# Optimization experiments

Hardware: AMD Instinct MI355X
Metric: run time of the kernel (lower is better)

The kernel has to match this reference:

```python
import jax, jax.numpy as jnp
import numpy as np

N, E, D, H, K = 100000, 1600000, 512, 256, 64


def setup_inputs() -> dict:
    key = jax.random.key(0)
    ks = jax.random.split(key, 8)
    x = jax.random.normal(ks[0], (N, D), dtype=jnp.float32)
    edge_index = jax.random.randint(ks[1], (2, E), 0, N, dtype=jnp.int64)
    W1 = jax.random.normal(ks[2], (D, H), dtype=jnp.float32) / np.sqrt(D)
    b1 = jnp.zeros((H,), dtype=jnp.float32)
    W2 = jax.random.normal(ks[3], (H, H), dtype=jnp.float32) / np.sqrt(H)
    b2 = jnp.zeros((H,), dtype=jnp.float32)
    Wk = jax.random.normal(ks[4], (H, K), dtype=jnp.float32) / np.sqrt(H)
    log_tau = jnp.array(np.log(1.0), dtype=jnp.float32)
    return {"x": x, "edge_index": edge_index, "W1": W1, "b1": b1,
            "W2": W2, "b2": b2, "Wk": Wk, "log_tau": log_tau}


def _gcn_norm(edge_index, n):
    # add self-loops, compute sym-normalized edge weights (PyG GCNConv default)
    loop = jnp.arange(n, dtype=edge_index.dtype)
    src = jnp.concatenate([edge_index[0], loop])
    dst = jnp.concatenate([edge_index[1], loop])
    deg = jax.ops.segment_sum(jnp.ones_like(dst, dtype=jnp.float32), dst, num_segments=n)
    dinv = jnp.where(deg > 0, jax.lax.rsqrt(deg), 0.0)
    norm = dinv[src] * dinv[dst]  # [E+N]
    return src, dst, norm


def _gcn_conv(h, W, b, src, dst, norm, n):
    hw = h @ W                      # dense GEMM [n, out]
    msg = hw[src] * norm[:, None]   # gather + scale
    out = jax.ops.segment_sum(msg, dst, num_segments=n)  # scatter-add
    return out + b


def reference(x, edge_index, W1, b1, W2, b2, Wk, log_tau):
    n = x.shape[0]
    src, dst, norm = _gcn_norm(edge_index, n)
    h = jax.nn.relu(_gcn_conv(x, W1, b1, src, dst, norm, n))
    h = _gcn_conv(h, W2, b2, src, dst, norm, n)
    logits = h @ Wk                 # [n, K]
    tau = jnp.exp(log_tau)
    S = jax.nn.softmax(logits / tau, axis=-1)
    return (S, logits)
```

## Files before the change

kernel.cpp:

```cpp
#include <hip/hip_runtime.h>

typedef unsigned short u16;
typedef unsigned int u32;

__device__ __forceinline__ float bfl(u32 u) { union { u32 i; float f; } v; v.i = u << 16; return v.f; }
__device__ __forceinline__ float bfh(u32 u) { union { u32 i; float f; } v; v.i = u & 0xffff0000u; return v.f; }
__device__ __forceinline__ float bf2f(u16 u) { union { u32 i; float f; } v; v.i = ((u32)u) << 16; return v.f; }
__device__ __forceinline__ u16 f2bf(float f) {
    union { float f; u32 i; } v; v.f = f;
    u32 r = v.i + 0x7fffu + ((v.i >> 16) & 1u);
    return (u16)(r >> 16);
}

typedef const __attribute__((address_space(1))) unsigned int* gas_u32;
typedef __attribute__((address_space(3))) unsigned int* las_u32;
__device__ __forceinline__ void async_cp16(const void* g, void* l) {
    __builtin_amdgcn_global_load_lds((gas_u32)g, (las_u32)l, 16, 0, 0);
}

__global__ void k_detect(const u32* __restrict__ xw, const int* __restrict__ eiw,
                         const void* __restrict__ ltau, int* __restrict__ flags,
                         int xwords, int E) {
    __shared__ int cf32, ci64nz;
    if (threadIdx.x == 0) { cf32 = 0; ci64nz = 0; }
    __syncthreads();
    int t = threadIdx.x;
    int xs = xwords / 256;
    u32 w = xw[(size_t)t * xs];
    int e = (int)((w >> 23) & 0xFFu);
    if (e >= 100 && e <= 140) atomicAdd(&cf32, 1);
    int es = E / 256;
    int hw = eiw[2 * (size_t)t * es + 1];
    if (hw != 0) atomicAdd(&ci64nz, 1);
    __syncthreads();
    if (t == 0) {
        int f32 = (cf32 >= 192) ? 1 : 0;
        flags[0] = f32;
        flags[1] = (ci64nz == 0) ? 1 : 0;
        ((float*)flags)[2] = f32 ? ((const float*)ltau)[0] : bf2f(((const u16*)ltau)[0]);
    }
}

__global__ void k_edges(const int* __restrict__ ei, int* __restrict__ src, int* __restrict__ dst,
                        int e, const int* __restrict__ flags) {
    int i = blockIdx.x * 256 + threadIdx.x;
    if (i >= e) return;
    if (flags[1]) { src[i] = ei[2 * i]; dst[i] = ei[2 * (e + i)]; }
    else          { src[i] = ei[i];     dst[i] = ei[e + i]; }
}

__global__ void k_deginit(int* deg, int n) {
    int i = blockIdx.x * 256 + threadIdx.x;
    if (i < n) deg[i] = 1;
}
__global__ void k_degcount(const int* __restrict__ dst, int* deg, int e) {
    int i = blockIdx.x * 256 + threadIdx.x;
    if (i < e) atomicAdd(&deg[dst[i]], 1);
}
__global__ void k_dinv(const int* __restrict__ deg, float* dinv, int n) {
    int i = blockIdx.x * 256 + threadIdx.x;
    if (i < n) dinv[i] = rsqrtf((float)deg[i]);
}
__global__ void k_blocksum(const int* __restrict__ deg, int* bsum, int n) {
    int b = blockIdx.x, t = threadIdx.x;
    int base = b * 1024 + t * 4;
    int s = 0;
#pragma unroll
    for (int j = 0; j < 4; j++) { int i = base + j; if (i < n) s += deg[i] - 1; }
    for (int d = 32; d; d >>= 1) s += __shfl_down(s, d);
    __shared__ int ws[4];
    int lane = t & 63, w = t >> 6;
    if (lane == 0) ws[w] = s;
    __syncthreads();
    if (t == 0) bsum[b] = ws[0] + ws[1] + ws[2] + ws[3];
}
__global__ void k_scanb(const int* __restrict__ bsum, int* boff, int nb, int* row_ptr, int n) {
    if (threadIdx.x == 0) {
        int acc = 0;
        for (int b = 0; b < nb; b++) { boff[b] = acc; acc += bsum[b]; }
        row_ptr[n] = acc;
    }
}
__global__ void k_scanwrite(const int* __restrict__ deg, const int* __restrict__ boff,
                            int* row_ptr, int* cursor, int n) {
    int b = blockIdx.x, t = threadIdx.x;
    int base = b * 1024 + t * 4;
    int v[4]; int s = 0;
#pragma unroll
    for (int j = 0; j < 4; j++) { int i = base + j; v[j] = (i < n) ? deg[i] - 1 : 0; s += v[j]; }
    int lane = t & 63, w = t >> 6;
    int inc = s;
    for (int d = 1; d < 64; d <<= 1) { int u = __shfl_up(inc, d); if (lane >= d) inc += u; }
    __shared__ int ws[4];
    if (lane == 63) ws[w] = inc;
    __syncthreads();
    int woff = 0;
    for (int i = 0; i < w; i++) woff += ws[i];
    int p = boff[b] + woff + inc - s;
#pragma unroll
    for (int j = 0; j < 4; j++) {
        int i = base + j;
        if (i < n) { row_ptr[i] = p; cursor[i] = p; p += v[j]; }
    }
}
__global__ void k_fill(const int* __restrict__ src, const int* __restrict__ dst,
                       int* cursor, int* col, int e) {
    int i = blockIdx.x * 256 + threadIdx.x;
    if (i < e) {
        int d = dst[i];
        int p = atomicAdd(&cursor[d], 1);
        col[p] = src[i];
    }
}
__global__ void k_transpose_flex(const void* __restrict__ in, u16* __restrict__ out,
                                 int R, int C, const int* __restrict__ flags) {
    int idx = blockIdx.x * 256 + threadIdx.x;
    if (idx >= R * C) return;
    u16 v = flags[0] ? f2bf(((const float*)in)[idx]) : ((const u16*)in)[idx];
    int r = idx / C, c = idx % C;
    out[(size_t)c * R + r] = v;
}

typedef __bf16 bf16x8 __attribute__((ext_vector_type(8)));
typedef float floatx4 __attribute__((ext_vector_type(4)));

template <int WROWS, int WCOLS, int TM, int TN, int MODE, bool AFLEX, bool OFLEX>
__global__ __launch_bounds__(256, 2) void k_gemm_bt(const void* __restrict__ A,
                                                    const u16* __restrict__ Bt,
                                                    void* __restrict__ C,
                                                    const float* __restrict__ dinv,
                                                    const int* __restrict__ flags,
                                                    long long obase,
                                                    int M, int Nd, int Kd) {
    constexpr int BM = WROWS * TM * 16;
    constexpr int BN = WCOLS * TN * 16;
    constexpr int BK = 32;
    __shared__ u16 As[2][BM][BK];
    __shared__ u16 Bs[2][BN][BK];
    const int af32 = AFLEX ? flags[0] : 0;
    const int of32 = OFLEX ? flags[0] : 0;
    const int tid = threadIdx.x;
    const int m0 = blockIdx.y * BM;
    const int n0 = blockIdx.x * BN;
    const int lane = tid & 63;
    const int wave = tid >> 6;
    const int wm = wave / WCOLS;
    const int wn = wave % WCOLS;
    const int mrow = lane & 15;
    const int quad = lane >> 4;

    floatx4 acc[TM][TN];
#pragma unroll
    for (int i = 0; i < TM; i++)
#pragma unroll
        for (int j = 0; j < TN; j++) { floatx4 z = {0.f, 0.f, 0.f, 0.f}; acc[i][j] = z; }

    auto stage = [&](int kk, int buf) {
        if (AFLEX && af32) {
#pragma unroll
            for (int idx = tid * 8; idx < BM * BK; idx += 256 * 8) {
                int r = idx >> 5, k = idx & 31;
                int gr = m0 + r;
                u16 t8[8] = {0, 0, 0, 0, 0, 0, 0, 0};
                if (gr < M) {
                    const float* ap = (const float*)A + (size_t)gr * Kd + kk + k;
                    float4 f0 = *(const float4*)ap;
                    float4 f1 = *(const float4*)(ap + 4);
                    t8[0] = f2bf(f0.x); t8[1] = f2bf(f0.y); t8[2] = f2bf(f0.z); t8[3] = f2bf(f0.w);
                    t8[4] = f2bf(f1.x); t8[5] = f2bf(f1.y); t8[6] = f2bf(f1.z); t8[7] = f2bf(f1.w);
                }
                *(int4*)&As[buf][r][k] = *(const int4*)t8;
            }
#pragma unroll
            for (int idx = tid * 8; idx < BN * BK; idx += 256 * 8) {
                int r = idx >> 5, k = idx & 31;
                int4 v = *(const int4*)(Bt + (size_t)(n0 + r) * Kd + kk + k);
                *(int4*)&Bs[buf][r][k] = v;
            }
        } else {
#pragma unroll
            for (int idx = tid * 8; idx < BM * BK; idx += 256 * 8) {
                int r = idx >> 5, k = idx & 31;
                int gr = m0 + r;
                if (gr >= M) gr = M - 1;
                async_cp16((const u16*)A + (size_t)gr * Kd + kk + k, &As[buf][r][k]);
            }
#pragma unroll
            for (int idx = tid * 8; idx < BN * BK; idx += 256 * 8) {
                int r = idx >> 5, k = idx & 31;
                async_cp16(Bt + (size_t)(n0 + r) * Kd + kk + k, &Bs[buf][r][k]);
            }
        }
    };

    const int steps = Kd / BK;
    stage(0, 0);
    for (int s = 0; s < steps; s++) {
        __syncthreads();
        if (s + 1 < steps) stage((s + 1) * BK, (s + 1) & 1);
        const int b = s & 1;
        bf16x8 af[TM], bfr[TN];
#pragma unroll
        for (int i = 0; i < TM; i++)
            af[i] = *(const bf16x8*)&As[b][wm * TM * 16 + i * 16 + mrow][quad * 8];
#pragma unroll
        for (int j = 0; j < TN; j++)
            bfr[j] = *(const bf16x8*)&Bs[b][wn * TN * 16 + j * 16 + mrow][quad * 8];
#pragma unroll
        for (int i = 0; i < TM; i++)
#pragma unroll
            for (int j = 0; j < TN; j++)
                acc[i][j] = __builtin_amdgcn_mfma_f32_16x16x32_bf16(af[i], bfr[j], acc[i][j], 0, 0, 0);
    }

#pragma unroll
    for (int i = 0; i < TM; i++) {
#pragma unroll
        for (int r = 0; r < 4; r++) {
            int grow = m0 + wm * TM * 16 + i * 16 + quad * 4 + r;
            if (grow < M) {
                float scale = (MODE == 0) ? dinv[grow] : 1.0f;
#pragma unroll
                for (int j = 0; j < TN; j++) {
                    int gcol = n0 + wn * TN * 16 + j * 16 + mrow;
                    float val = acc[i][j][r] * scale;
                    long long cidx = obase + (long long)grow * Nd + gcol;
                    if (OFLEX && of32) ((float*)C)[cidx] = val;
                    else               ((u16*)C)[cidx] = f2bf(val);
                }
            }
        }
    }
}

__global__ __launch_bounds__(256) void k_agg(const u16* __restrict__ g, u16* __restrict__ out,
                                             const int* __restrict__ row_ptr,
                                             const int* __restrict__ col,
                                             const float* __restrict__ dinv,
                                             const void* __restrict__ bias,
                                             const int* __restrict__ flags,
                                             int n, int do_relu) {
    int wid = (int)((blockIdx.x * 256 + threadIdx.x) >> 6);
    int lane = threadIdx.x & 63;
    if (wid >= n) return;
    const u16* gp = g + (size_t)lane * 4;
    uint2 rv = *(const uint2*)(gp + (size_t)wid * 256);
    float a0 = bfl(rv.x), a1 = bfh(rv.x), a2 = bfl(rv.y), a3 = bfh(rv.y);
    int beg = row_ptr[wid], end = row_ptr[wid + 1];
    for (int base = beg; base < end; base += 64) {
        int m = end - base; if (m > 64) m = 64;
        int ci = (base + lane < end) ? col[base + lane] : 0;
        int j = 0;
        for (; j + 8 <= m; j += 8) {
            uint2 v[8];
#pragma unroll
            for (int q = 0; q < 8; q++) {
                int s = __shfl(ci, j + q);
                v[q] = *(const uint2*)(gp + (size_t)s * 256);
            }
#pragma unroll
            for (int q = 0; q < 8; q++) {
                a0 += bfl(v[q].x); a1 += bfh(v[q].x);
                a2 += bfl(v[q].y); a3 += bfh(v[q].y);
            }
        }
        for (; j < m; j++) {
            int s = __shfl(ci, j);
            uint2 v = *(const uint2*)(gp + (size_t)s * 256);
            a0 += bfl(v.x); a1 += bfh(v.x); a2 += bfl(v.y); a3 += bfh(v.y);
        }
    }
    float dv = dinv[wid];
    float b0, b1, b2, b3;
    if (flags[0]) {
        float4 q = ((const float4*)bias)[lane];
        b0 = q.x; b1 = q.y; b2 = q.z; b3 = q.w;
    } else {
        uint2 bv = ((const uint2*)bias)[lane];
        b0 = bfl(bv.x); b1 = bfh(bv.x); b2 = bfl(bv.y); b3 = bfh(bv.y);
    }
    a0 = a0 * dv + b0;
    a1 = a1 * dv + b1;
    a2 = a2 * dv + b2;
    a3 = a3 * dv + b3;
    if (do_relu) {
        a0 = fmaxf(a0, 0.f); a1 = fmaxf(a1, 0.f); a2 = fmaxf(a2, 0.f); a3 = fmaxf(a3, 0.f);
    }
    uint2 o;
    o.x = (u32)f2bf(a0) | ((u32)f2bf(a1) << 16);
    o.y = (u32)f2bf(a2) | ((u32)f2bf(a3) << 16);
    *(uint2*)(out + (size_t)wid * 256 + (size_t)lane * 4) = o;
}

__global__ __launch_bounds__(256) void k_softmax(void* __restrict__ out, long long NK,
                                                 const int* __restrict__ flags, int n) {
    int wid = (int)((blockIdx.x * 256 + threadIdx.x) >> 6);
    int lane = threadIdx.x & 63;
    if (wid >= n) return;
    int f32o = flags[0];
    float lt = ((const float*)flags)[2];
    float inv_tau = __expf(-lt);
    long long li = NK + (long long)wid * 64 + lane;
    float x = f32o ? ((const float*)out)[li] : bf2f(((const u16*)out)[li]);
    x *= inv_tau;
    float m = x;
    for (int d = 32; d; d >>= 1) m = fmaxf(m, __shfl_xor(m, d));
    float e = __expf(x - m);
    float s = e;
    for (int d = 32; d; d >>= 1) s += __shfl_xor(s, d);
    float r = e / s;
    long long si = (long long)wid * 64 + lane;
    if (f32o) ((float*)out)[si] = r;
    else      ((u16*)out)[si] = f2bf(r);
}

extern "C" void kernel_launch(void* const* d_in, const int* in_sizes, int n_in,
                              void* d_out, int out_size, void* d_ws, size_t ws_size,
                              hipStream_t stream) {
    const void* x    = d_in[0];
    const int*  ei   = (const int*)d_in[1];
    const void* W1   = d_in[2];
    const void* b1   = d_in[3];
    const void* W2   = d_in[4];
    const void* b2   = d_in[5];
    const void* Wk   = d_in[6];
    const void* ltau = d_in[7];
    const int D = 512, H = 256, K = 64;
    const int N = in_sizes[0] / D;
    const int E = in_sizes[1] / 2;
    const long long NK = (long long)N * K;

    u16* g = (u16*)d_ws;
    u16* h = g + (size_t)N * H;
    int* flags = (int*)(h + (size_t)N * H);
    int* srcv = (int*)g;
    int* dstv = srcv + E;

    size_t ooff = 0;
    auto oalloc = [&](size_t bytes) -> char* {
        char* p = (char*)d_out + ooff;
        ooff += (bytes + 255) & ~(size_t)255;
        return p;
    };
    int*   col     = (int*)oalloc((size_t)E * 4);
    int*   deg     = (int*)oalloc((size_t)N * 4);
    float* dinv    = (float*)oalloc((size_t)N * 4);
    int*   row_ptr = (int*)oalloc((size_t)(N + 1) * 4);
    int*   cursor  = (int*)oalloc((size_t)N * 4);
    int*   bsum    = (int*)oalloc(1024);
    int*   boff    = (int*)oalloc(1024);
    u16*   W1t     = (u16*)oalloc((size_t)D * H * 2);
    u16*   W2t     = (u16*)oalloc((size_t)H * H * 2);
    u16*   Wkt     = (u16*)oalloc((size_t)H * K * 2);

    const int nb = (N + 1023) / 1024;
    auto g256 = [](long long n) { return (int)((n + 255) / 256); };

    k_detect<<<1, 256, 0, stream>>>((const u32*)x, ei, ltau, flags, in_sizes[0] / 2, E);
    k_edges<<<g256(E), 256, 0, stream>>>(ei, srcv, dstv, E, flags);
    k_deginit<<<g256(N), 256, 0, stream>>>(deg, N);
    k_degcount<<<g256(E), 256, 0, stream>>>(dstv, deg, E);
    k_dinv<<<g256(N), 256, 0, stream>>>(deg, dinv, N);
    k_blocksum<<<nb, 256, 0, stream>>>(deg, bsum, N);
    k_scanb<<<1, 64, 0, stream>>>(bsum, boff, nb, row_ptr, N);
    k_scanwrite<<<nb, 256, 0, stream>>>(deg, boff, row_ptr, cursor, N);
    k_fill<<<g256(E), 256, 0, stream>>>(srcv, dstv, cursor, col, E);

    k_transpose_flex<<<g256((long long)D * H), 256, 0, stream>>>(W1, W1t, D, H, flags);
    k_transpose_flex<<<g256((long long)H * H), 256, 0, stream>>>(W2, W2t, H, H, flags);
    k_transpose_flex<<<g256((long long)H * K), 256, 0, stream>>>(Wk, Wkt, H, K, flags);

    const int mtiles = (N + 127) / 128;
    k_gemm_bt<2, 2, 4, 8, 0, true, false>
        <<<dim3(1, mtiles), 256, 0, stream>>>(x, W1t, g, dinv, flags, 0, N, H, D);
    k_agg<<<g256((long long)N * 64), 256, 0, stream>>>(g, h, row_ptr, col, dinv, b1, flags, N, 1);
    k_gemm_bt<2, 2, 4, 8, 0, false, false>
        <<<dim3(1, mtiles), 256, 0, stream>>>(h, W2t, g, dinv, flags, 0, N, H, H);
    k_agg<<<g256((long long)N * 64), 256, 0, stream>>>(g, h, row_ptr, col, dinv, b2, flags, N, 0);
    k_gemm_bt<4, 1, 2, 4, 1, false, true>
        <<<dim3(1, mtiles), 256, 0, stream>>>(h, Wkt, d_out, dinv, flags, NK, N, K, H);
    k_softmax<<<g256((long long)N * 64), 256, 0, stream>>>(d_out, NK, flags, N);
}
```

Before: 870.4 us.

## Build CSR via two-level bucketed counting sort and retile GEMMs to 64 rows

Replaces the per-node global atomic degree count, multi-kernel scan and random atomic fill with a bucketed counting sort. Edges are first binned into 128-node buckets using shared-memory histograms and packed as (local dst, src) words, then each bucket block builds its row_ptr, dinv and col entries locally with shared atomics. The aim is to cut contention on global atomics and scattered writes, at the cost of an extra edge buffer pass and a cap on nb (1024 buckets) and on src width (25 bits). Separately, the GEMMs use 64-row tiles with a 1x4 wave layout and launch bounds of 4 to raise occupancy.

```diff
diff --git a/kernel.cpp b/kernel.cpp
--- a/kernel.cpp
+++ b/kernel.cpp
@@ -49,69 +49,120 @@
     else          { src[i] = ei[i];     dst[i] = ei[e + i]; }
 }
 
-__global__ void k_deginit(int* deg, int n) {
+__global__ void k_zeroi(int* p, int n) {
     int i = blockIdx.x * 256 + threadIdx.x;
-    if (i < n) deg[i] = 1;
-}
-__global__ void k_degcount(const int* __restrict__ dst, int* deg, int e) {
-    int i = blockIdx.x * 256 + threadIdx.x;
-    if (i < e) atomicAdd(&deg[dst[i]], 1);
-}
-__global__ void k_dinv(const int* __restrict__ deg, float* dinv, int n) {
-    int i = blockIdx.x * 256 + threadIdx.x;
-    if (i < n) dinv[i] = rsqrtf((float)deg[i]);
-}
-__global__ void k_blocksum(const int* __restrict__ deg, int* bsum, int n) {
-    int b = blockIdx.x, t = threadIdx.x;
-    int base = b * 1024 + t * 4;
+    if (i < n) p[i] = 0;
+}
+
+__global__ __launch_bounds__(256) void k_bcount(const int* __restrict__ dst, int* __restrict__ bcount,
+                                                int e, int nb) {
+    __shared__ int h[1024];
+    int t = threadIdx.x;
+    for (int i = t; i < nb; i += 256) h[i] = 0;
+    __syncthreads();
+    int chunk = (e + gridDim.x - 1) / gridDim.x;
+    int beg = blockIdx.x * chunk;
+    int end = beg + chunk; if (end > e) end = e;
+    for (int i = beg + t; i < end; i += 256) atomicAdd(&h[dst[i] >> 7], 1);
+    __syncthreads();
+    for (int i = t; i < nb; i += 256) { int v = h[i]; if (v) atomicAdd(&bcount[i], v); }
+}
+
+__global__ __launch_bounds__(1024) void k_bscan(const int* __restrict__ bcount, int* __restrict__ bbase,
+                                                int* __restrict__ bcursor, int nb) {
+    int t = threadIdx.x;
+    int per = (nb + 1023) >> 10;
+    int b0 = t * per;
+    int ls[8];
     int s = 0;
 #pragma unroll
-    for (int j = 0; j < 4; j++) { int i = base + j; if (i < n) s += deg[i] - 1; }
-    for (int d = 32; d; d >>= 1) s += __shfl_down(s, d);
-    __shared__ int ws[4];
-    int lane = t & 63, w = t >> 6;
-    if (lane == 0) ws[w] = s;
-    __syncthreads();
-    if (t == 0) bsum[b] = ws[0] + ws[1] + ws[2] + ws[3];
-}
-__global__ void k_scanb(const int* __restrict__ bsum, int* boff, int nb, int* row_ptr, int n) {
-    if (threadIdx.x == 0) {
-        int acc = 0;
-        for (int b = 0; b < nb; b++) { boff[b] = acc; acc += bsum[b]; }
-        row_ptr[n] = acc;
-    }
-}
-__global__ void k_scanwrite(const int* __restrict__ deg, const int* __restrict__ boff,
-                            int* row_ptr, int* cursor, int n) {
-    int b = blockIdx.x, t = threadIdx.x;
-    int base = b * 1024 + t * 4;
-    int v[4]; int s = 0;
-#pragma unroll
-    for (int j = 0; j < 4; j++) { int i = base + j; v[j] = (i < n) ? deg[i] - 1 : 0; s += v[j]; }
+    for (int j = 0; j < 8; j++) {
+        int v = 0;
+        if (j < per && b0 + j < nb) v = bcount[b0 + j];
+        ls[j] = v; s += v;
+    }
     int lane = t & 63, w = t >> 6;
     int inc = s;
     for (int d = 1; d < 64; d <<= 1) { int u = __shfl_up(inc, d); if (lane >= d) inc += u; }
-    __shared__ int ws[4];
-    if (lane == 63) ws[w] = inc;
-    __syncthreads();
-    int woff = 0;
-    for (int i = 0; i < w; i++) woff += ws[i];
-    int p = boff[b] + woff + inc - s;
-#pragma unroll
-    for (int j = 0; j < 4; j++) {
-        int i = base + j;
-        if (i < n) { row_ptr[i] = p; cursor[i] = p; p += v[j]; }
-    }
-}
-__global__ void k_fill(const int* __restrict__ src, const int* __restrict__ dst,
-                       int* cursor, int* col, int e) {
-    int i = blockIdx.x * 256 + threadIdx.x;
-    if (i < e) {
+    __shared__ int wsum[16];
+    __shared__ int gtot;
+    if (lane == 63) wsum[w] = inc;
+    __syncthreads();
+    if (t == 0) { int a = 0; for (int i = 0; i < 16; i++) { int x = wsum[i]; wsum[i] = a; a += x; } gtot = a; }
+    __syncthreads();
+    int base = wsum[w] + inc - s;
+#pragma unroll
+    for (int j = 0; j < 8; j++) {
+        if (j < per && b0 + j < nb) { bbase[b0 + j] = base; bcursor[b0 + j] = base; base += ls[j]; }
+    }
+    if (t == 0) bbase[nb] = gtot;
+}
+
+__global__ __launch_bounds__(256) void k_bscatter(const int* __restrict__ src, const int* __restrict__ dst,
+                                                  int* __restrict__ bcursor, u32* __restrict__ ebuf,
+                                                  int e, int nb) {
+    __shared__ int h[1024];
+    __shared__ int lbase[1024];
+    int t = threadIdx.x;
+    for (int i = t; i < nb; i += 256) h[i] = 0;
+    __syncthreads();
+    int chunk = (e + gridDim.x - 1) / gridDim.x;
+    int beg = blockIdx.x * chunk;
+    int end = beg + chunk; if (end > e) end = e;
+    for (int i = beg + t; i < end; i += 256) atomicAdd(&h[dst[i] >> 7], 1);
+    __syncthreads();
+    for (int i = t; i < nb; i += 256) {
+        int v = h[i];
+        lbase[i] = v ? atomicAdd(&bcursor[i], v) : 0;
+        h[i] = 0;
+    }
+    __syncthreads();
+    for (int i = beg + t; i < end; i += 256) {
         int d = dst[i];
-        int p = atomicAdd(&cursor[d], 1);
-        col[p] = src[i];
-    }
-}
+        int b = d >> 7;
+        int p = lbase[b] + atomicAdd(&h[b], 1);
+        ebuf[p] = ((u32)(d & 127) << 25) | (u32)src[i];
+    }
+}
+
+__global__ __launch_bounds__(256) void k_bcsr(const u32* __restrict__ ebuf, const int* __restrict__ bbase,
+                                              int* __restrict__ row_ptr, float* __restrict__ dinv,
+                                              int* __restrict__ col, int n, int nb, int e) {
+    __shared__ int hist[128], sc[128], cur[128];
+    int b = blockIdx.x, t = threadIdx.x;
+    if (t < 128) hist[t] = 0;
+    __syncthreads();
+    int beg = bbase[b], end = bbase[b + 1];
+    for (int j = beg + t; j < end; j += 256) atomicAdd(&hist[ebuf[j] >> 25], 1);
+    __syncthreads();
+    if (t < 128) sc[t] = hist[t];
+    __syncthreads();
+    for (int d = 1; d < 128; d <<= 1) {
+        int v = 0;
+        if (t < 128 && t >= d) v = sc[t - d];
+        __syncthreads();
+        if (t < 128) sc[t] += v;
+        __syncthreads();
+    }
+    if (t < 128) {
+        int node = (b << 7) + t;
+        if (node < n) {
+            int ex = sc[t] - hist[t];
+            row_ptr[node] = beg + ex;
+            dinv[node] = rsqrtf((float)(hist[t] + 1));
+            cur[t] = ex;
+        }
+    }
+    if (b == 0 && t == 0) row_ptr[n] = e;
+    __syncthreads();
+    for (int j = beg + t; j < end; j += 256) {
+        u32 ev = ebuf[j];
+        int dl = (int)(ev >> 25);
+        int p = atomicAdd(&cur[dl], 1);
+        col[beg + p] = (int)(ev & 0x1FFFFFFu);
+    }
+}
+
 __global__ void k_transpose_flex(const void* __restrict__ in, u16* __restrict__ out,
                                  int R, int C, const int* __restrict__ flags) {
     int idx = blockIdx.x * 256 + threadIdx.x;
@@ -125,7 +176,7 @@
 typedef float floatx4 __attribute__((ext_vector_type(4)));
 
 template <int WROWS, int WCOLS, int TM, int TN, int MODE, bool AFLEX, bool OFLEX>
-__global__ __launch_bounds__(256, 2) void k_gemm_bt(const void* __restrict__ A,
+__global__ __launch_bounds__(256, 4) void k_gemm_bt(const void* __restrict__ A,
                                                     const u16* __restrict__ Bt,
                                                     void* __restrict__ C,
                                                     const float* __restrict__ dinv,
@@ -329,12 +380,14 @@
     const int N = in_sizes[0] / D;
     const int E = in_sizes[1] / 2;
     const long long NK = (long long)N * K;
+    const int nb = (N + 127) >> 7;
 
     u16* g = (u16*)d_ws;
     u16* h = g + (size_t)N * H;
     int* flags = (int*)(h + (size_t)N * H);
     int* srcv = (int*)g;
     int* dstv = srcv + E;
+    u32* ebuf = (u32*)(dstv + E);
 
     size_t ooff = 0;
     auto oalloc = [&](size_t bytes) -> char* {
@@ -343,41 +396,37 @@
         return p;
     };
     int*   col     = (int*)oalloc((size_t)E * 4);
-    int*   deg     = (int*)oalloc((size_t)N * 4);
     float* dinv    = (float*)oalloc((size_t)N * 4);
     int*   row_ptr = (int*)oalloc((size_t)(N + 1) * 4);
-    int*   cursor  = (int*)oalloc((size_t)N * 4);
-    int*   bsum    = (int*)oalloc(1024);
-    int*   boff    = (int*)oalloc(1024);
+    int*   bcount  = (int*)oalloc((size_t)nb * 4);
+    int*   bbase   = (int*)oalloc((size_t)(nb + 1) * 4);
+    int*   bcursor = (int*)oalloc((size_t)nb * 4);
     u16*   W1t     = (u16*)oalloc((size_t)D * H * 2);
     u16*   W2t     = (u16*)oalloc((size_t)H * H * 2);
     u16*   Wkt     = (u16*)oalloc((size_t)H * K * 2);
 
-    const int nb = (N + 1023) / 1024;
     auto g256 = [](long long n) { return (int)((n + 255) / 256); };
 
     k_detect<<<1, 256, 0, stream>>>((const u32*)x, ei, ltau, flags, in_sizes[0] / 2, E);
     k_edges<<<g256(E), 256, 0, stream>>>(ei, srcv, dstv, E, flags);
-    k_deginit<<<g256(N), 256, 0, stream>>>(deg, N);
-    k_degcount<<<g256(E), 256, 0, stream>>>(dstv, deg, E);
-    k_dinv<<<g256(N), 256, 0, stream>>>(deg, dinv, N);
-    k_blocksum<<<nb, 256, 0, stream>>>(deg, bsum, N);
-    k_scanb<<<1, 64, 0, stream>>>(bsum, boff, nb, row_ptr, N);
-    k_scanwrite<<<nb, 256, 0, stream>>>(deg, boff, row_ptr, cursor, N);
-    k_fill<<<g256(E), 256, 0, stream>>>(srcv, dstv, cursor, col, E);
+    k_zeroi<<<g256(nb), 256, 0, stream>>>(bcount, nb);
+    k_bcount<<<256, 256, 0, stream>>>(dstv, bcount, E, nb);
+    k_bscan<<<1, 1024, 0, stream>>>(bcount, bbase, bcursor, nb);
+    k_bscatter<<<256, 256, 0, stream>>>(srcv, dstv, bcursor, ebuf, E, nb);
+    k_bcsr<<<nb, 256, 0, stream>>>(ebuf, bbase, row_ptr, dinv, col, N, nb, E);
 
     k_transpose_flex<<<g256((long long)D * H), 256, 0, stream>>>(W1, W1t, D, H, flags);
     k_transpose_flex<<<g256((long long)H * H), 256, 0, stream>>>(W2, W2t, H, H, flags);
     k_transpose_flex<<<g256((long long)H * K), 256, 0, stream>>>(Wk, Wkt, H, K, flags);
 
-    const int mtiles = (N + 127) / 128;
-    k_gemm_bt<2, 2, 4, 8, 0, true, false>
-        <<<dim3(1, mtiles), 256, 0, stream>>>(x, W1t, g, dinv, flags, 0, N, H, D);
+    const int m64 = (N + 63) / 64;
+    k_gemm_bt<1, 4, 4, 4, 0, true, false>
+        <<<dim3(1, m64), 256, 0, stream>>>(x, W1t, g, dinv, flags, 0, N, H, D);
     k_agg<<<g256((long long)N * 64), 256, 0, stream>>>(g, h, row_ptr, col, dinv, b1, flags, N, 1);
-    k_gemm_bt<2, 2, 4, 8, 0, false, false>
-        <<<dim3(1, mtiles), 256, 0, stream>>>(h, W2t, g, dinv, flags, 0, N, H, H);
+    k_gemm_bt<1, 4, 4, 4, 0, false, false>
+        <<<dim3(1, m64), 256, 0, stream>>>(h, W2t, g, dinv, flags, 0, N, H, H);
     k_agg<<<g256((long long)N * 64), 256, 0, stream>>>(g, h, row_ptr, col, dinv, b2, flags, N, 0);
-    k_gemm_bt<4, 1, 2, 4, 1, false, true>
-        <<<dim3(1, mtiles), 256, 0, stream>>>(h, Wkt, d_out, dinv, flags, NK, N, K, H);
+    k_gemm_bt<1, 4, 4, 1, 1, false, true>
+        <<<dim3(1, m64), 256, 0, stream>>>(h, Wkt, d_out, dinv, flags, NK, N, K, H);
     k_softmax<<<g256((long long)N * 64), 256, 0, stream>>>(d_out, NK, flags, N);
 }
```

New measurement: 709.7 us. -18.5%, faster.
